# Kernel tuning notes

Measured on AMD Instinct MI355X. Metric: run time of the kernel, lower is better.

The kernel has to match this reference:

```python
import jax, jax.numpy as jnp
import numpy as np

NUM_HEADS = 8
MAX_REL = 32  # max_relative_positions
LN_EPS = 1e-5


def _conv1x1(x, W, b):
    # x: (B, C, H, W), W: (Cout, Cin), b: (Cout,)
    return jnp.einsum('bchw,oc->bohw', x, W) + b[None, :, None, None]


def setup_inputs() -> dict:
    key = jax.random.key(0)
    ks = jax.random.split(key, 10)
    B, C, H, W = 2, 512, 48, 48
    L = H * W
    s = 1.0 / np.sqrt(C)
    inp = {
        'x': jax.random.normal(ks[0], (B, C, H, W), jnp.float32),
        'mask': jax.random.randint(ks[1], (1, NUM_HEADS, L, L), 0, 2).astype(bool),
        'learnable_pos': jax.random.normal(ks[2], (1, C, H, W), jnp.float32) * 0.02,
        'Wq': jax.random.normal(ks[3], (C, C), jnp.float32) * s,
        'bq': jnp.zeros((C,), jnp.float32),
        'Wk': jax.random.normal(ks[4], (C, C), jnp.float32) * s,
        'bk': jnp.zeros((C,), jnp.float32),
        'Wv': jax.random.normal(ks[5], (C, C), jnp.float32) * s,
        'bv': jnp.zeros((C,), jnp.float32),
        'Wo': jax.random.normal(ks[6], (C, C), jnp.float32) * s,
        'bo': jnp.zeros((C,), jnp.float32),
        'rel_table': jax.random.normal(ks[7], (NUM_HEADS, 2 * MAX_REL + 1), jnp.float32) * 0.02,
        'ln_gamma': jnp.ones((C,), jnp.float32),
        'ln_beta': jnp.zeros((C,), jnp.float32),
    }
    return inp


def reference(x, mask, learnable_pos, Wq, bq, Wk, bk, Wv, bv, Wo, bo,
              rel_table, ln_gamma, ln_beta):
    B, C, H, W = x.shape
    L = H * W
    hd = C // NUM_HEADS
    residual = x

    xp = x + learnable_pos
    q = _conv1x1(xp, Wq, bq)
    k = _conv1x1(xp, Wk, bk)
    v = _conv1x1(xp, Wv, bv)

    def split_heads(t):  # (B,C,H,W) -> (B, heads, L, hd)
        return t.reshape(B, NUM_HEADS, hd, L).transpose(0, 1, 3, 2)

    q, k, v = split_heads(q), split_heads(k), split_heads(v)

    scale = 1.0 / np.sqrt(hd).astype(np.float32)
    scores = jnp.einsum('bhld,bhmd->bhlm', q, k) * scale  # (B,H,L,L)

    # relative positional bias per head
    pos = jnp.arange(L)
    rp = jnp.clip(pos[:, None] - pos[None, :], -MAX_REL, MAX_REL) + MAX_REL  # (L,L)
    scores = scores + rel_table[:, rp][None]  # (1,heads,L,L) broadcast

    scores = jnp.where(mask, scores, jnp.float32(-1e9))
    attn = jax.nn.softmax(scores, axis=-1)

    out = jnp.einsum('bhlm,bhmd->bhld', attn, v)  # (B,heads,L,hd)
    out = out.transpose(0, 1, 3, 2).reshape(B, C, H, W)
    out = _conv1x1(out, Wo, bo)

    y = residual + out
    # LayerNorm over channels (channels-last permute in original)
    yl = y.transpose(0, 2, 3, 1)  # (B,H,W,C)
    mu = jnp.mean(yl, axis=-1, keepdims=True)
    var = jnp.var(yl, axis=-1, keepdims=True)
    yl = (yl - mu) * jax.lax.rsqrt(var + LN_EPS) * ln_gamma + ln_beta
    return yl.transpose(0, 3, 1, 2)
```

## Files before the change

kernel.cpp:

```cpp
#include <hip/hip_runtime.h>
#include <cstdint>

#define L_SEQ 2304
#define CDIM  512
#define NHEADS 8
#define HD    64
#define LL    ((size_t)L_SEQ * L_SEQ)
#define ROWS_TOT (16 * L_SEQ)
#define PERBL ((size_t)2 * L_SEQ * 512)

typedef short  s8v  __attribute__((ext_vector_type(8)));
typedef float  f4v  __attribute__((ext_vector_type(4)));

__device__ __forceinline__ ushort f2bf(float f) {
    union { float f; uint32_t u; } v; v.f = f;
    uint32_t u = v.u;
    uint32_t r = (u + 0x7FFFu + ((u >> 16) & 1u)) >> 16;
    return (ushort)r;
}

__device__ __forceinline__ float bf2f(ushort u) {
    union { uint32_t u; float f; } v; v.u = (uint32_t)u << 16;
    return v.f;
}

__global__ __launch_bounds__(256) void prep(
    const float* __restrict__ Wq, const float* __restrict__ Wk,
    const float* __restrict__ Wv, const float* __restrict__ Wo,
    const float* __restrict__ x, const float* __restrict__ pos,
    ushort* __restrict__ wf, ushort* __restrict__ xt)
{
    __shared__ ushort T[64][72];
    const int bx = blockIdx.x;
    const int t  = threadIdx.x;
    if (bx < 512) {
        const int i    = bx * 256 + t;
        const int lane = i & 63;
        const int F    = (i >> 6) & 63;
        const int ob   = (i >> 12) & 7;
        const int mat  = i >> 15;
        const float* src = (mat == 0) ? Wq : (mat == 1) ? Wk : (mat == 2) ? Wv : Wo;
        const int row = ob * 64 + (F & 3) * 16 + (lane & 15);
        const int col = (F >> 2) * 32 + (lane >> 4) * 8;
        const float4 w0 = *(const float4*)&src[(size_t)row * 512 + col];
        const float4 w1 = *(const float4*)&src[(size_t)row * 512 + col + 4];
        ushort4 o0, o1;
        o0.x = f2bf(w0.x); o0.y = f2bf(w0.y); o0.z = f2bf(w0.z); o0.w = f2bf(w0.w);
        o1.x = f2bf(w1.x); o1.y = f2bf(w1.y); o1.z = f2bf(w1.z); o1.w = f2bf(w1.w);
        *(ushort4*)&wf[(size_t)i * 8]     = o0;
        *(ushort4*)&wf[(size_t)i * 8 + 4] = o1;
    } else {
        const int bb = bx - 512;
        const int l0 = (bb % 36) * 64;
        const int c0 = ((bb / 36) & 7) * 64;
        const int b  = bb / 288;
        const int cc = t >> 2;
        const int l4 = (t & 3) * 16;
        const size_t off  = ((size_t)b * CDIM + c0 + cc) * L_SEQ + l0 + l4;
        const size_t poff = (size_t)(c0 + cc) * L_SEQ + l0 + l4;
        #pragma unroll
        for (int j4 = 0; j4 < 4; j4++) {
            const float4 xv = *(const float4*)&x[off + j4 * 4];
            const float4 pv = *(const float4*)&pos[poff + j4 * 4];
            T[cc][l4 + j4 * 4 + 0] = f2bf(xv.x + pv.x);
            T[cc][l4 + j4 * 4 + 1] = f2bf(xv.y + pv.y);
            T[cc][l4 + j4 * 4 + 2] = f2bf(xv.z + pv.z);
            T[cc][l4 + j4 * 4 + 3] = f2bf(xv.w + pv.w);
        }
        __syncthreads();
        const int lr = t >> 2;
        const int c4 = (t & 3) * 16;
        ushort o[16];
        #pragma unroll
        for (int j = 0; j < 16; j++) o[j] = T[c4 + j][lr];
        ushort* dst = &xt[((size_t)b * L_SEQ + l0 + lr) * 512 + c0 + c4];
        *(ushort4*)&dst[0]  = *(ushort4*)&o[0];
        *(ushort4*)&dst[4]  = *(ushort4*)&o[4];
        *(ushort4*)&dst[8]  = *(ushort4*)&o[8];
        *(ushort4*)&dst[12] = *(ushort4*)&o[12];
    }
}

__global__ __launch_bounds__(256) void qkv_mfma(
    const ushort* __restrict__ xt, const ushort* __restrict__ wf,
    const float* __restrict__ bq, const float* __restrict__ bk,
    const float* __restrict__ bv,
    ushort* __restrict__ q_t, ushort* __restrict__ k_t, ushort* __restrict__ v_t)
{
    const int l0 = blockIdx.x * 64;
    const int ob = blockIdx.y;
    const int o0 = ob * 64;
    const int b  = blockIdx.z;
    const int t = threadIdx.x, w = t >> 6, lane = t & 63;
    const int n16 = lane & 15, q4 = lane >> 4;

    const ushort* A = xt + ((size_t)b * L_SEQ + l0 + w * 16 + n16) * 512 + q4 * 8;

    s8v areg[16];
    #pragma unroll
    for (int i = 0; i < 16; i++) areg[i] = *(const s8v*)&A[i * 32];

    const size_t lb = (size_t)lane * 8;

    f4v acc[3][4] = {};
    for (int ks = 0; ks < 16; ks++) {
        s8v bf[3][4];
        #pragma unroll
        for (int m = 0; m < 3; m++)
            #pragma unroll
            for (int t4 = 0; t4 < 4; t4++)
                bf[m][t4] = *(const s8v*)&wf[
                    ((size_t)((m * 8 + ob) * 64 + ks * 4 + t4)) * 512 + lb];
        const s8v a = areg[ks];
        #pragma unroll
        for (int m = 0; m < 3; m++)
            #pragma unroll
            for (int t4 = 0; t4 < 4; t4++)
                acc[m][t4] = __builtin_amdgcn_mfma_f32_16x16x32_bf16(a, bf[m][t4], acc[m][t4], 0, 0, 0);
    }

    const int h = ob;
    const int rowbase = l0 + w * 16 + q4 * 4;

    #pragma unroll
    for (int m = 0; m < 2; m++) {
        const float* bias = (m == 0) ? bq : bk;
        const float sc = (m == 0) ? 0.125f : 1.0f;
        ushort* op = (m == 0 ? q_t : k_t) + ((size_t)(b * NHEADS + h)) * L_SEQ * HD;
        #pragma unroll
        for (int t4 = 0; t4 < 4; t4++) {
            const float bi = bias[o0 + t4 * 16 + n16];
            #pragma unroll
            for (int r = 0; r < 4; r++)
                op[(size_t)(rowbase + r) * HD + t4 * 16 + n16] = f2bf((acc[m][t4][r] + bi) * sc);
        }
    }
    {
        ushort* op = v_t + ((size_t)(b * NHEADS + h)) * HD * L_SEQ;
        #pragma unroll
        for (int t4 = 0; t4 < 4; t4++) {
            const float bi = bv[o0 + t4 * 16 + n16];
            ushort4 st;
            st.x = f2bf(acc[2][t4][0] + bi);
            st.y = f2bf(acc[2][t4][1] + bi);
            st.z = f2bf(acc[2][t4][2] + bi);
            st.w = f2bf(acc[2][t4][3] + bi);
            *(ushort4*)&op[(size_t)(t4 * 16 + n16) * L_SEQ + rowbase] = st;
        }
    }
}

__global__ __launch_bounds__(256) void flash_attn_mfma(
    const ushort* __restrict__ q, const ushort* __restrict__ k,
    const ushort* __restrict__ vt, const int* __restrict__ mask,
    const float* __restrict__ rel_table, ushort* __restrict__ Opart,
    float* __restrict__ Lpart)
{
    __shared__ __align__(16) ushort Kf[512 * 8];
    __shared__ __align__(16) ushort Vf[512 * 8];
    __shared__ __align__(16) ushort Pb[4 * 16 * 72];
    __shared__ float rt[65];

    const int t    = threadIdx.x;
    const int id   = blockIdx.x;
    const int h    = id & 7;
    const int s2   = id >> 3;
    const int b    = s2 & 1;
    const int half = (s2 >> 1) & 1;
    const int qb   = s2 >> 2;
    const int bh   = b * NHEADS + h;
    const int l0   = qb * 64;
    const int w    = t >> 6;
    const int lane = t & 63;
    const int n16  = lane & 15;
    const int q4   = lane >> 4;

    if (t < 65) rt[t] = rel_table[h * 65 + t];

    const ushort* qp = q  + (size_t)bh * L_SEQ * HD;
    const ushort* kp = k  + (size_t)bh * L_SEQ * HD;
    const ushort* vp = vt + (size_t)bh * HD * L_SEQ;
    const int*    mp = mask + (size_t)h * LL;

    const int qrow = l0 + w * 16 + n16;
    const s8v qA0 = *(const s8v*)&qp[(size_t)qrow * HD + q4 * 8];
    const s8v qA1 = *(const s8v*)&qp[(size_t)qrow * HD + 32 + q4 * 8];

    f4v O[4] = {{0.f,0.f,0.f,0.f},{0.f,0.f,0.f,0.f},{0.f,0.f,0.f,0.f},{0.f,0.f,0.f,0.f}};
    float lrun[4] = {0.f, 0.f, 0.f, 0.f};

    int sKey[2], sD0[2], sDd[2];
    #pragma unroll
    for (int cc = 0; cc < 2; cc++) {
        const int c = t + cc * 256;
        const int g = c >> 6;
        const int sT = g >> 1, sS = g & 1;
        const int sQ = (c >> 4) & 3, sN = c & 15;
        sKey[cc] = sT * 16 + sN;
        sD0[cc]  = sS * 32 + sQ * 8;
        sDd[cc]  = sT * 16 + sN;
    }

    const int rowbase = l0 + w * 16 + q4 * 4;
    const int kbase = half * 1152;

    s8v kreg[2], vreg[2];
    int mreg[4][4];
    #pragma unroll
    for (int cc = 0; cc < 2; cc++) {
        kreg[cc] = *(const s8v*)&kp[(size_t)(kbase + sKey[cc]) * HD + sD0[cc]];
        vreg[cc] = *(const s8v*)&vp[(size_t)sDd[cc] * L_SEQ + kbase + sD0[cc]];
    }
    #pragma unroll
    for (int t4 = 0; t4 < 4; t4++)
        #pragma unroll
        for (int r = 0; r < 4; r++)
            mreg[t4][r] = mp[(size_t)(rowbase + r) * L_SEQ + kbase + t4 * 16 + n16];

    for (int mt = 0; mt < 18; mt++) {
        const int mb = kbase + mt * 64;
        __syncthreads();
        #pragma unroll
        for (int cc = 0; cc < 2; cc++) {
            const int c = t + cc * 256;
            *(s8v*)&Kf[c * 8] = kreg[cc];
            *(s8v*)&Vf[c * 8] = vreg[cc];
        }
        __syncthreads();

        const int mb2 = (mt < 17) ? mb + 64 : mb;
        s8v knx[2], vnx[2];
        int mnx[4][4];
        #pragma unroll
        for (int cc = 0; cc < 2; cc++) {
            knx[cc] = *(const s8v*)&kp[(size_t)(mb2 + sKey[cc]) * HD + sD0[cc]];
            vnx[cc] = *(const s8v*)&vp[(size_t)sDd[cc] * L_SEQ + mb2 + sD0[cc]];
        }
        #pragma unroll
        for (int t4 = 0; t4 < 4; t4++)
            #pragma unroll
            for (int r = 0; r < 4; r++)
                mnx[t4][r] = mp[(size_t)(rowbase + r) * L_SEQ + mb2 + t4 * 16 + n16];

        f4v S[4];
        #pragma unroll
        for (int t4 = 0; t4 < 4; t4++) {
            const s8v b0 = *(const s8v*)&Kf[((t4 * 2 + 0) * 64 + lane) * 8];
            const s8v b1 = *(const s8v*)&Kf[((t4 * 2 + 1) * 64 + lane) * 8];
            f4v acc = {0.f, 0.f, 0.f, 0.f};
            acc = __builtin_amdgcn_mfma_f32_16x16x32_bf16(qA0, b0, acc, 0, 0, 0);
            acc = __builtin_amdgcn_mfma_f32_16x16x32_bf16(qA1, b1, acc, 0, 0, 0);
            S[t4] = acc;
        }

        #pragma unroll
        for (int t4 = 0; t4 < 4; t4++) {
            const int A = (l0 + w * 16) - (mb + t4 * 16);
            if (A >= 47) {
                const float bu = rt[64];
                #pragma unroll
                for (int r = 0; r < 4; r++) S[t4][r] += bu;
            } else if (A <= -47) {
                const float bu = rt[0];
                #pragma unroll
                for (int r = 0; r < 4; r++) S[t4][r] += bu;
            } else {
                #pragma unroll
                for (int r = 0; r < 4; r++) {
                    int dix = A + q4 * 4 + r - n16;
                    dix = min(max(dix, -32), 32) + 32;
                    S[t4][r] += rt[dix];
                }
            }
            #pragma unroll
            for (int r = 0; r < 4; r++)
                if (mreg[t4][r] == 0) S[t4][r] = -1e9f;
        }

        float sum[4] = {0.f, 0.f, 0.f, 0.f};
        #pragma unroll
        for (int r = 0; r < 4; r++) {
            #pragma unroll
            for (int t4 = 0; t4 < 4; t4++) {
                const float p = __expf(S[t4][r]);
                sum[r] += p;
                Pb[w * 1152 + (q4 * 4 + r) * 72 + t4 * 16 + n16] = f2bf(p);
            }
        }

        const s8v pf0 = *(const s8v*)&Pb[w * 1152 + n16 * 72 + q4 * 8];
        const s8v pf1 = *(const s8v*)&Pb[w * 1152 + n16 * 72 + 32 + q4 * 8];
        #pragma unroll
        for (int t4 = 0; t4 < 4; t4++) {
            f4v o = O[t4];
            const s8v v0 = *(const s8v*)&Vf[((t4 * 2 + 0) * 64 + lane) * 8];
            const s8v v1 = *(const s8v*)&Vf[((t4 * 2 + 1) * 64 + lane) * 8];
            o = __builtin_amdgcn_mfma_f32_16x16x32_bf16(pf0, v0, o, 0, 0, 0);
            o = __builtin_amdgcn_mfma_f32_16x16x32_bf16(pf1, v1, o, 0, 0, 0);
            O[t4] = o;
        }

        #pragma unroll
        for (int r = 0; r < 4; r++) {
            float s = sum[r];
            s += __shfl_xor(s, 1);
            s += __shfl_xor(s, 2);
            s += __shfl_xor(s, 4);
            s += __shfl_xor(s, 8);
            lrun[r] += s;
        }

        #pragma unroll
        for (int cc = 0; cc < 2; cc++) { kreg[cc] = knx[cc]; vreg[cc] = vnx[cc]; }
        #pragma unroll
        for (int t4 = 0; t4 < 4; t4++)
            #pragma unroll
            for (int r = 0; r < 4; r++)
                mreg[t4][r] = mnx[t4][r];
    }

    ushort* op = Opart + (size_t)half * PERBL + (size_t)b * L_SEQ * 512;
    #pragma unroll
    for (int r = 0; r < 4; r++) {
        const size_t base = (size_t)(rowbase + r) * 512 + h * 64;
        #pragma unroll
        for (int t4 = 0; t4 < 4; t4++)
            op[base + t4 * 16 + n16] = f2bf(O[t4][r]);
    }
    if (n16 == 0) {
        const size_t sb = (size_t)half * ROWS_TOT + (size_t)bh * L_SEQ;
        #pragma unroll
        for (int r = 0; r < 4; r++)
            Lpart[sb + rowbase + r] = lrun[r];
    }
}

__global__ __launch_bounds__(256) void out_mfma(
    const ushort* __restrict__ Opart, const float* __restrict__ Lp,
    const ushort* __restrict__ wf, const float* __restrict__ bo,
    const float* __restrict__ x, float* __restrict__ y)
{
    const int l0 = blockIdx.x * 64;
    const int ob = blockIdx.y;
    const int o0 = ob * 64;
    const int b  = blockIdx.z;
    const int t = threadIdx.x, w = t >> 6, lane = t & 63;
    const int n16 = lane & 15, q4 = lane >> 4;

    const int l = l0 + w * 16 + n16;

    float fsc[8];
    #pragma unroll
    for (int h = 0; h < 8; h++) {
        const size_t s = (size_t)(b * NHEADS + h) * L_SEQ + l;
        fsc[h] = 1.0f / (Lp[s] + Lp[ROWS_TOT + s]);
    }

    const ushort* o0p = Opart + ((size_t)b * L_SEQ + l) * 512 + q4 * 8;
    const ushort* o1p = o0p + PERBL;

    s8v areg[16];
    #pragma unroll
    for (int ks = 0; ks < 16; ks++) {
        const ushort4 a0 = *(const ushort4*)&o0p[ks * 32];
        const ushort4 a1 = *(const ushort4*)&o0p[ks * 32 + 4];
        const ushort4 c0 = *(const ushort4*)&o1p[ks * 32];
        const ushort4 c1 = *(const ushort4*)&o1p[ks * 32 + 4];
        const float f = fsc[ks >> 1];
        s8v a;
        a[0] = (short)f2bf((bf2f(a0.x) + bf2f(c0.x)) * f);
        a[1] = (short)f2bf((bf2f(a0.y) + bf2f(c0.y)) * f);
        a[2] = (short)f2bf((bf2f(a0.z) + bf2f(c0.z)) * f);
        a[3] = (short)f2bf((bf2f(a0.w) + bf2f(c0.w)) * f);
        a[4] = (short)f2bf((bf2f(a1.x) + bf2f(c1.x)) * f);
        a[5] = (short)f2bf((bf2f(a1.y) + bf2f(c1.y)) * f);
        a[6] = (short)f2bf((bf2f(a1.z) + bf2f(c1.z)) * f);
        a[7] = (short)f2bf((bf2f(a1.w) + bf2f(c1.w)) * f);
        areg[ks] = a;
    }

    const size_t lb = (size_t)lane * 8;

    f4v acc[4] = {{0.f,0.f,0.f,0.f},{0.f,0.f,0.f,0.f},{0.f,0.f,0.f,0.f},{0.f,0.f,0.f,0.f}};
    for (int ks = 0; ks < 16; ks++) {
        s8v bf[4];
        #pragma unroll
        for (int t4 = 0; t4 < 4; t4++)
            bf[t4] = *(const s8v*)&wf[
                ((size_t)((3 * 8 + ob) * 64 + ks * 4 + t4)) * 512 + lb];
        const s8v a = areg[ks];
        #pragma unroll
        for (int t4 = 0; t4 < 4; t4++)
            acc[t4] = __builtin_amdgcn_mfma_f32_16x16x32_bf16(a, bf[t4], acc[t4], 0, 0, 0);
    }

    const int rowbase = l0 + w * 16 + q4 * 4;
    #pragma unroll
    for (int t4 = 0; t4 < 4; t4++) {
        const int o = o0 + t4 * 16 + n16;
        const float bi = bo[o];
        const size_t off = ((size_t)b * CDIM + o) * L_SEQ + rowbase;
        const float4 xv = *(const float4*)&x[off];
        float4 st;
        st.x = acc[t4][0] + bi + xv.x;
        st.y = acc[t4][1] + bi + xv.y;
        st.z = acc[t4][2] + bi + xv.z;
        st.w = acc[t4][3] + bi + xv.w;
        *(float4*)&y[off] = st;
    }
}

__global__ __launch_bounds__(256) void ln_kernel(
    float* __restrict__ y, const float* __restrict__ gamma,
    const float* __restrict__ beta)
{
    const int t = threadIdx.x;
    const int p = t & 31;
    const int g = t >> 5;
    const int pos = blockIdx.x * 32 + p;
    const int b = (pos >= L_SEQ) ? 1 : 0;
    const int l = pos - b * L_SEQ;
    float* col = y + (size_t)b * CDIM * L_SEQ + l;

    float s = 0.f, sq = 0.f;
    for (int c = g * 64; c < g * 64 + 64; c++) {
        const float v = col[(size_t)c * L_SEQ];
        s += v; sq += v * v;
    }
    __shared__ float S1[8][32];
    __shared__ float S2[8][32];
    S1[g][p] = s; S2[g][p] = sq;
    __syncthreads();
    if (t < 32) {
        float ss = 0.f, qq = 0.f;
        #pragma unroll
        for (int gg = 0; gg < 8; gg++) { ss += S1[gg][t]; qq += S2[gg][t]; }
        const float mu = ss * (1.0f / CDIM);
        const float var = qq * (1.0f / CDIM) - mu * mu;
        S1[0][t] = mu;
        S2[0][t] = rsqrtf(var + 1e-5f);
    }
    __syncthreads();
    const float mu = S1[0][p];
    const float rs = S2[0][p];
    for (int c = g * 64; c < g * 64 + 64; c++) {
        const float v = col[(size_t)c * L_SEQ];
        col[(size_t)c * L_SEQ] = (v - mu) * rs * gamma[c] + beta[c];
    }
}

extern "C" void kernel_launch(void* const* d_in, const int* in_sizes, int n_in,
                              void* d_out, int out_size, void* d_ws, size_t ws_size,
                              hipStream_t stream) {
    const float* x    = (const float*)d_in[0];
    const int* mask   = (const int*)d_in[1];
    const float* pos  = (const float*)d_in[2];
    const float* Wq   = (const float*)d_in[3];
    const float* bq   = (const float*)d_in[4];
    const float* Wk   = (const float*)d_in[5];
    const float* bk   = (const float*)d_in[6];
    const float* Wv   = (const float*)d_in[7];
    const float* bv   = (const float*)d_in[8];
    const float* Wo   = (const float*)d_in[9];
    const float* bo   = (const float*)d_in[10];
    const float* rel  = (const float*)d_in[11];
    const float* gam  = (const float*)d_in[12];
    const float* bet  = (const float*)d_in[13];

    ushort* qw  = (ushort*)d_ws;
    ushort* kw  = qw + PERBL;
    ushort* vw  = kw + PERBL;
    ushort* xtw = vw + PERBL;
    ushort* wbw = xtw + PERBL;
    ushort* Opart = wbw + (size_t)4 * 262144;
    float* Lpart = (float*)(Opart + 2 * PERBL);
    float* y = (float*)d_out;

    prep<<<dim3(512 + 576), 256, 0, stream>>>(Wq, Wk, Wv, Wo, x, pos, wbw, xtw);

    qkv_mfma<<<dim3(L_SEQ / 64, CDIM / 64, 2), 256, 0, stream>>>(
        xtw, wbw, bq, bk, bv, qw, kw, vw);

    flash_attn_mfma<<<dim3(1152), 256, 0, stream>>>(qw, kw, vw, mask, rel,
                                                    Opart, Lpart);

    out_mfma<<<dim3(L_SEQ / 64, CDIM / 64, 2), 256, 0, stream>>>(
        Opart, Lpart, wbw, bo, x, y);

    ln_kernel<<<(2 * L_SEQ) / 32, 256, 0, stream>>>(y, gam, bet);
}
```

Baseline: 365.6 us.

## Process two 16-row query groups per wave to reuse K/V tiles

Each wave in the flash attention kernel now handles 32 query rows as two 16-row groups, so each block covers 128 query rows and the grid halves to 576 blocks. K and V tiles loaded into shared memory are reused across twice as many queries, which cuts global K/V traffic and barrier count per query. The cost is higher register pressure (double O accumulators, mask registers, Q fragments) and fewer blocks, which can reduce occupancy on the 256-CU device.

```diff
diff --git a/kernel.cpp b/kernel.cpp
--- a/kernel.cpp
+++ b/kernel.cpp
@@ -169,7 +169,7 @@
     const int half = (s2 >> 1) & 1;
     const int qb   = s2 >> 2;
     const int bh   = b * NHEADS + h;
-    const int l0   = qb * 64;
+    const int l0   = qb * 128;
     const int w    = t >> 6;
     const int lane = t & 63;
     const int n16  = lane & 15;
@@ -182,12 +182,16 @@
     const ushort* vp = vt + (size_t)bh * HD * L_SEQ;
     const int*    mp = mask + (size_t)h * LL;
 
-    const int qrow = l0 + w * 16 + n16;
-    const s8v qA0 = *(const s8v*)&qp[(size_t)qrow * HD + q4 * 8];
-    const s8v qA1 = *(const s8v*)&qp[(size_t)qrow * HD + 32 + q4 * 8];
-
-    f4v O[4] = {{0.f,0.f,0.f,0.f},{0.f,0.f,0.f,0.f},{0.f,0.f,0.f,0.f},{0.f,0.f,0.f,0.f}};
-    float lrun[4] = {0.f, 0.f, 0.f, 0.f};
+    s8v qA[2][2];
+    #pragma unroll
+    for (int rg = 0; rg < 2; rg++) {
+        const int qrow = l0 + w * 32 + rg * 16 + n16;
+        qA[rg][0] = *(const s8v*)&qp[(size_t)qrow * HD + q4 * 8];
+        qA[rg][1] = *(const s8v*)&qp[(size_t)qrow * HD + 32 + q4 * 8];
+    }
+
+    f4v O[2][4] = {};
+    float lrun[2][4] = {};
 
     int sKey[2], sD0[2], sDd[2];
     #pragma unroll
@@ -201,21 +205,25 @@
         sDd[cc]  = sT * 16 + sN;
     }
 
-    const int rowbase = l0 + w * 16 + q4 * 4;
+    int rowbase[2];
+    #pragma unroll
+    for (int rg = 0; rg < 2; rg++) rowbase[rg] = l0 + w * 32 + rg * 16 + q4 * 4;
     const int kbase = half * 1152;
 
     s8v kreg[2], vreg[2];
-    int mreg[4][4];
+    int mreg[2][4][4];
     #pragma unroll
     for (int cc = 0; cc < 2; cc++) {
         kreg[cc] = *(const s8v*)&kp[(size_t)(kbase + sKey[cc]) * HD + sD0[cc]];
         vreg[cc] = *(const s8v*)&vp[(size_t)sDd[cc] * L_SEQ + kbase + sD0[cc]];
     }
     #pragma unroll
-    for (int t4 = 0; t4 < 4; t4++)
-        #pragma unroll
-        for (int r = 0; r < 4; r++)
-            mreg[t4][r] = mp[(size_t)(rowbase + r) * L_SEQ + kbase + t4 * 16 + n16];
+    for (int rg = 0; rg < 2; rg++)
+        #pragma unroll
+        for (int t4 = 0; t4 < 4; t4++)
+            #pragma unroll
+            for (int r = 0; r < 4; r++)
+                mreg[rg][t4][r] = mp[(size_t)(rowbase[rg] + r) * L_SEQ + kbase + t4 * 16 + n16];
 
     for (int mt = 0; mt < 18; mt++) {
         const int mb = kbase + mt * 64;
@@ -230,108 +238,118 @@
 
         const int mb2 = (mt < 17) ? mb + 64 : mb;
         s8v knx[2], vnx[2];
-        int mnx[4][4];
+        int mnx[2][4][4];
         #pragma unroll
         for (int cc = 0; cc < 2; cc++) {
             knx[cc] = *(const s8v*)&kp[(size_t)(mb2 + sKey[cc]) * HD + sD0[cc]];
             vnx[cc] = *(const s8v*)&vp[(size_t)sDd[cc] * L_SEQ + mb2 + sD0[cc]];
         }
         #pragma unroll
-        for (int t4 = 0; t4 < 4; t4++)
-            #pragma unroll
-            for (int r = 0; r < 4; r++)
-                mnx[t4][r] = mp[(size_t)(rowbase + r) * L_SEQ + mb2 + t4 * 16 + n16];
-
-        f4v S[4];
-        #pragma unroll
-        for (int t4 = 0; t4 < 4; t4++) {
-            const s8v b0 = *(const s8v*)&Kf[((t4 * 2 + 0) * 64 + lane) * 8];
-            const s8v b1 = *(const s8v*)&Kf[((t4 * 2 + 1) * 64 + lane) * 8];
-            f4v acc = {0.f, 0.f, 0.f, 0.f};
-            acc = __builtin_amdgcn_mfma_f32_16x16x32_bf16(qA0, b0, acc, 0, 0, 0);
-            acc = __builtin_amdgcn_mfma_f32_16x16x32_bf16(qA1, b1, acc, 0, 0, 0);
-            S[t4] = acc;
-        }
-
-        #pragma unroll
-        for (int t4 = 0; t4 < 4; t4++) {
-            const int A = (l0 + w * 16) - (mb + t4 * 16);
-            if (A >= 47) {
-                const float bu = rt[64];
+        for (int rg = 0; rg < 2; rg++)
+            #pragma unroll
+            for (int t4 = 0; t4 < 4; t4++)
                 #pragma unroll
-                for (int r = 0; r < 4; r++) S[t4][r] += bu;
-            } else if (A <= -47) {
-                const float bu = rt[0];
+                for (int r = 0; r < 4; r++)
+                    mnx[rg][t4][r] = mp[(size_t)(rowbase[rg] + r) * L_SEQ + mb2 + t4 * 16 + n16];
+
+        #pragma unroll
+        for (int rg = 0; rg < 2; rg++) {
+            f4v S[4];
+            #pragma unroll
+            for (int t4 = 0; t4 < 4; t4++) {
+                const s8v b0 = *(const s8v*)&Kf[((t4 * 2 + 0) * 64 + lane) * 8];
+                const s8v b1 = *(const s8v*)&Kf[((t4 * 2 + 1) * 64 + lane) * 8];
+                f4v acc = {0.f, 0.f, 0.f, 0.f};
+                acc = __builtin_amdgcn_mfma_f32_16x16x32_bf16(qA[rg][0], b0, acc, 0, 0, 0);
+                acc = __builtin_amdgcn_mfma_f32_16x16x32_bf16(qA[rg][1], b1, acc, 0, 0, 0);
+                S[t4] = acc;
+            }
+
+            #pragma unroll
+            for (int t4 = 0; t4 < 4; t4++) {
+                const int A = (l0 + w * 32 + rg * 16) - (mb + t4 * 16);
+                if (A >= 47) {
+                    const float bu = rt[64];
+                    #pragma unroll
+                    for (int r = 0; r < 4; r++) S[t4][r] += bu;
+                } else if (A <= -47) {
+                    const float bu = rt[0];
+                    #pragma unroll
+                    for (int r = 0; r < 4; r++) S[t4][r] += bu;
+                } else {
+                    #pragma unroll
+                    for (int r = 0; r < 4; r++) {
+                        int dix = A + q4 * 4 + r - n16;
+                        dix = min(max(dix, -32), 32) + 32;
+                        S[t4][r] += rt[dix];
+                    }
+                }
                 #pragma unroll
-                for (int r = 0; r < 4; r++) S[t4][r] += bu;
-            } else {
+                for (int r = 0; r < 4; r++)
+                    if (mreg[rg][t4][r] == 0) S[t4][r] = -1e9f;
+            }
+
+            float sum[4] = {0.f, 0.f, 0.f, 0.f};
+            #pragma unroll
+            for (int r = 0; r < 4; r++) {
                 #pragma unroll
-                for (int r = 0; r < 4; r++) {
-                    int dix = A + q4 * 4 + r - n16;
-                    dix = min(max(dix, -32), 32) + 32;
-                    S[t4][r] += rt[dix];
+                for (int t4 = 0; t4 < 4; t4++) {
+                    const float p = __expf(S[t4][r]);
+                    sum[r] += p;
+                    Pb[w * 1152 + (q4 * 4 + r) * 72 + t4 * 16 + n16] = f2bf(p);
                 }
             }
+
+            const s8v pf0 = *(const s8v*)&Pb[w * 1152 + n16 * 72 + q4 * 8];
+            const s8v pf1 = *(const s8v*)&Pb[w * 1152 + n16 * 72 + 32 + q4 * 8];
+            #pragma unroll
+            for (int t4 = 0; t4 < 4; t4++) {
+                f4v o = O[rg][t4];
+                const s8v v0 = *(const s8v*)&Vf[((t4 * 2 + 0) * 64 + lane) * 8];
+                const s8v v1 = *(const s8v*)&Vf[((t4 * 2 + 1) * 64 + lane) * 8];
+                o = __builtin_amdgcn_mfma_f32_16x16x32_bf16(pf0, v0, o, 0, 0, 0);
+                o = __builtin_amdgcn_mfma_f32_16x16x32_bf16(pf1, v1, o, 0, 0, 0);
+                O[rg][t4] = o;
+            }
+
+            #pragma unroll
+            for (int r = 0; r < 4; r++) {
+                float s = sum[r];
+                s += __shfl_xor(s, 1);
+                s += __shfl_xor(s, 2);
+                s += __shfl_xor(s, 4);
+                s += __shfl_xor(s, 8);
+                lrun[rg][r] += s;
+            }
+        }
+
+        #pragma unroll
+        for (int cc = 0; cc < 2; cc++) { kreg[cc] = knx[cc]; vreg[cc] = vnx[cc]; }
+        #pragma unroll
+        for (int rg = 0; rg < 2; rg++)
+            #pragma unroll
+            for (int t4 = 0; t4 < 4; t4++)
+                #pragma unroll
+                for (int r = 0; r < 4; r++)
+                    mreg[rg][t4][r] = mnx[rg][t4][r];
+    }
+
+    ushort* op = Opart + (size_t)half * PERBL + (size_t)b * L_SEQ * 512;
+    #pragma unroll
+    for (int rg = 0; rg < 2; rg++) {
+        #pragma unroll
+        for (int r = 0; r < 4; r++) {
+            const size_t base = (size_t)(rowbase[rg] + r) * 512 + h * 64;
+            #pragma unroll
+            for (int t4 = 0; t4 < 4; t4++)
+                op[base + t4 * 16 + n16] = f2bf(O[rg][t4][r]);
+        }
+        if (n16 == 0) {
+            const size_t sb = (size_t)half * ROWS_TOT + (size_t)bh * L_SEQ;
             #pragma unroll
             for (int r = 0; r < 4; r++)
-                if (mreg[t4][r] == 0) S[t4][r] = -1e9f;
-        }
-
-        float sum[4] = {0.f, 0.f, 0.f, 0.f};
-        #pragma unroll
-        for (int r = 0; r < 4; r++) {
-            #pragma unroll
-            for (int t4 = 0; t4 < 4; t4++) {
-                const float p = __expf(S[t4][r]);
-                sum[r] += p;
-                Pb[w * 1152 + (q4 * 4 + r) * 72 + t4 * 16 + n16] = f2bf(p);
-            }
-        }
-
-        const s8v pf0 = *(const s8v*)&Pb[w * 1152 + n16 * 72 + q4 * 8];
-        const s8v pf1 = *(const s8v*)&Pb[w * 1152 + n16 * 72 + 32 + q4 * 8];
-        #pragma unroll
-        for (int t4 = 0; t4 < 4; t4++) {
-            f4v o = O[t4];
-            const s8v v0 = *(const s8v*)&Vf[((t4 * 2 + 0) * 64 + lane) * 8];
-            const s8v v1 = *(const s8v*)&Vf[((t4 * 2 + 1) * 64 + lane) * 8];
-            o = __builtin_amdgcn_mfma_f32_16x16x32_bf16(pf0, v0, o, 0, 0, 0);
-            o = __builtin_amdgcn_mfma_f32_16x16x32_bf16(pf1, v1, o, 0, 0, 0);
-            O[t4] = o;
-        }
-
-        #pragma unroll
-        for (int r = 0; r < 4; r++) {
-            float s = sum[r];
-            s += __shfl_xor(s, 1);
-            s += __shfl_xor(s, 2);
-            s += __shfl_xor(s, 4);
-            s += __shfl_xor(s, 8);
-            lrun[r] += s;
-        }
-
-        #pragma unroll
-        for (int cc = 0; cc < 2; cc++) { kreg[cc] = knx[cc]; vreg[cc] = vnx[cc]; }
-        #pragma unroll
-        for (int t4 = 0; t4 < 4; t4++)
-            #pragma unroll
-            for (int r = 0; r < 4; r++)
-                mreg[t4][r] = mnx[t4][r];
-    }
-
-    ushort* op = Opart + (size_t)half * PERBL + (size_t)b * L_SEQ * 512;
-    #pragma unroll
-    for (int r = 0; r < 4; r++) {
-        const size_t base = (size_t)(rowbase + r) * 512 + h * 64;
-        #pragma unroll
-        for (int t4 = 0; t4 < 4; t4++)
-            op[base + t4 * 16 + n16] = f2bf(O[t4][r]);
-    }
-    if (n16 == 0) {
-        const size_t sb = (size_t)half * ROWS_TOT + (size_t)bh * L_SEQ;
-        #pragma unroll
-        for (int r = 0; r < 4; r++)
-            Lpart[sb + rowbase + r] = lrun[r];
+                Lpart[sb + rowbase[rg] + r] = lrun[rg][r];
+        }
     }
 }
 
@@ -481,8 +499,8 @@
     qkv_mfma<<<dim3(L_SEQ / 64, CDIM / 64, 2), 256, 0, stream>>>(
         xtw, wbw, bq, bk, bv, qw, kw, vw);
 
-    flash_attn_mfma<<<dim3(1152), 256, 0, stream>>>(qw, kw, vw, mask, rel,
-                                                    Opart, Lpart);
+    flash_attn_mfma<<<dim3(576), 256, 0, stream>>>(qw, kw, vw, mask, rel,
+                                                   Opart, Lpart);
 
     out_mfma<<<dim3(L_SEQ / 64, CDIM / 64, 2), 256, 0, stream>>>(
         Opart, Lpart, wbw, bo, x, y);
```

After: 388.2 us. 6.2% more time.
